# Performance work log

Measured on AMD Instinct MI355X. Metric: run time of the kernel, lower is better.

Reference implementation:

```python
import jax, jax.numpy as jnp
import numpy as np
import math

B, D_MODEL, H, D_K, L = 24, 128, 8, 16, 512


def setup_inputs() -> dict:
    key = jax.random.key(0)
    ks = jax.random.split(key, 5)
    x = jax.random.normal(ks[0], (B, D_MODEL, L), dtype=jnp.float32)
    Wq = jax.random.normal(ks[1], (H, B, D_K, D_MODEL), dtype=jnp.float32)
    Wk = jax.random.normal(ks[2], (H, B, D_K, D_MODEL), dtype=jnp.float32)
    Wv = jax.random.normal(ks[3], (H, B, D_K, D_MODEL), dtype=jnp.float32)
    Wo = jax.random.normal(ks[4], (B, H * D_K, D_MODEL), dtype=jnp.float32)
    return {"x": x, "Wq": Wq, "Wk": Wk, "Wv": Wv, "Wo": Wo}


def reference(x, Wq, Wk, Wv, Wo):
    # Per-head, per-batch projections: [h,b,k,d] @ [b,d,l] -> [h,b,k,l]
    Q = jnp.einsum('hbkd,bdl->hbkl', Wq, x)
    K = jnp.einsum('hbkd,bdl->hbkl', Wk, x)
    V = jnp.einsum('hbkd,bdl->hbkl', Wv, x)
    # scores[h,b,l,m] = Q[:, :, :, l] . K[:, :, :, m]; torch softmax dim=1 of
    # the [B, L, L] score -> softmax over the QUERY axis l (axis=2 here).
    scores = jnp.einsum('hbkl,hbkm->hblm', Q, K) / math.sqrt(D_K)
    attn = jax.nn.softmax(scores, axis=2)
    # head_i = V @ attn : [h,b,v,l] @ [h,b,l,m] -> [h,b,v,m]
    heads = jnp.einsum('hbvl,hblm->hbvm', V, attn)
    # concat heads along channel dim: [b, h*v, L]
    head = heads.transpose(1, 0, 2, 3).reshape(B, H * D_K, L)
    # out = Wo @ head : [b, h*v, d_model] treated as [b,128,128] @ [b,128,L]
    out = jnp.einsum('bod,bdl->bol', Wo, head)
    return out
```

## Files before the change

kernel.cpp:

```cpp
#include <hip/hip_runtime.h>
#include <math.h>

#define NB 24
#define DM 128
#define NH 8
#define DK 16
#define LL 512
#define HB (NH * NB)

#define XTH_OFF 0
#define XTL_OFF 3145728
#define HT_OFF  6291456

typedef __attribute__((ext_vector_type(8))) short bf16x8;
typedef __attribute__((ext_vector_type(4))) float f32x4;
typedef __attribute__((ext_vector_type(4))) int   i32x4;

#define MFMA  __builtin_amdgcn_mfma_f32_16x16x32_bf16
#define EXP2  __builtin_amdgcn_exp2f
#define BPERM __builtin_amdgcn_ds_bpermute

static __device__ __forceinline__ unsigned bfr(float x) {
    return (__float_as_uint(x) + 0x8000u) & 0xffff0000u;
}

static __device__ __forceinline__ unsigned cvtpk(float a, float b) {
    unsigned r;
    asm("v_cvt_pk_bf16_f32 %0, %1, %2" : "=v"(r) : "v"(a), "v"(b));
    return r;
}

static __device__ __forceinline__ void wsplit(const float* __restrict__ p,
                                              bf16x8& aH, bf16x8& aL) {
    const float4 f0 = *(const float4*)p;
    const float4 f1 = *(const float4*)(p + 4);
    const float f[8] = {f0.x, f0.y, f0.z, f0.w, f1.x, f1.y, f1.z, f1.w};
    i32x4 h, l;
    #pragma unroll
    for (int q = 0; q < 4; ++q) {
        const unsigned h0 = bfr(f[2 * q]), h1 = bfr(f[2 * q + 1]);
        const unsigned e0 = bfr(f[2 * q]     - __uint_as_float(h0));
        const unsigned e1 = bfr(f[2 * q + 1] - __uint_as_float(h1));
        h[q] = (int)((h0 >> 16) | (h1 & 0xffff0000u));
        l[q] = (int)((e0 >> 16) | (e1 & 0xffff0000u));
    }
    aH = __builtin_bit_cast(bf16x8, h);
    aL = __builtin_bit_cast(bf16x8, l);
}

__global__ __launch_bounds__(256)
void prep(const float* __restrict__ x,
          unsigned short* __restrict__ xthi,
          unsigned short* __restrict__ xtlo)
{
    __shared__ float T[64][65];
    const int bid = blockIdx.x, tid = threadIdx.x;
    const int b = bid >> 3, lc = bid & 7;

    #pragma unroll
    for (int half = 0; half < 2; ++half) {
        const int d0 = half << 6;
        const float* __restrict__ xb =
            x + (size_t)b * 65536 + (size_t)d0 * LL + lc * 64;
        if (half) __syncthreads();
        #pragma unroll
        for (int i = 0; i < 16; ++i) {
            const int idx = i * 256 + tid;
            T[idx >> 6][idx & 63] = xb[(size_t)(idx >> 6) * LL + (idx & 63)];
        }
        __syncthreads();
        #pragma unroll
        for (int i = 0; i < 8; ++i) {
            const int idx = (i * 256 + tid) * 2;
            const int l = idx >> 6, dd = idx & 63;
            const float v0 = T[dd][l], v1 = T[dd + 1][l];
            const unsigned h0 = bfr(v0), h1 = bfr(v1);
            const unsigned e0 = bfr(v0 - __uint_as_float(h0));
            const unsigned e1 = bfr(v1 - __uint_as_float(h1));
            const size_t o = (size_t)b * 65536 +
                             (size_t)(lc * 64 + l) * DM + d0 + dd;
            *(unsigned*)(xthi + o) = (h0 >> 16) | (h1 & 0xffff0000u);
            *(unsigned*)(xtlo + o) = (e0 >> 16) | (e1 & 0xffff0000u);
        }
    }
}

static __device__ __forceinline__ void pv_acc(
    const f32x4& s0, const f32x4& s1, float M, float& sm,
    f32x4& O, const bf16x8& aV, int addr0, int addr1, bool up, bool odd16)
{
    const float e0 = EXP2(s0[0] - M), e1 = EXP2(s0[1] - M);
    const float e2 = EXP2(s0[2] - M), e3 = EXP2(s0[3] - M);
    const float e4 = EXP2(s1[0] - M), e5 = EXP2(s1[1] - M);
    const float e6 = EXP2(s1[2] - M), e7 = EXP2(s1[3] - M);
    sm += ((e0 + e1) + (e2 + e3)) + ((e4 + e5) + (e6 + e7));
    const unsigned c0 = cvtpk(e0, e1), c1 = cvtpk(e2, e3);
    const unsigned c2 = cvtpk(e4, e5), c3 = cvtpk(e6, e7);
    const int r0 = (int)(odd16 ? c2 : c0);
    const int r1 = (int)(odd16 ? c0 : c2);
    const int r2 = (int)(odd16 ? c3 : c1);
    const int r3 = (int)(odd16 ? c1 : c3);
    const int w0 = BPERM(addr0, r0);
    const int w1 = BPERM(addr1, r1);
    const int w2 = BPERM(addr0, r2);
    const int w3 = BPERM(addr1, r3);
    i32x4 bi = { up ? w0 : w1, up ? w2 : w3,
                 up ? w1 : w0, up ? w3 : w2 };
    O = MFMA(aV, __builtin_bit_cast(bf16x8, bi), O, 0, 0, 0);
}

#define QK_STRIDE 40
#define V_STRIDE  520

__global__ __launch_bounds__(512)
void qkv_attn(const unsigned short* __restrict__ xthi,
              const unsigned short* __restrict__ xtlo,
              const float* __restrict__ Wq,
              const float* __restrict__ Wk,
              const float* __restrict__ Wv,
              unsigned short* __restrict__ ht)
{
    __shared__ unsigned short qs[LL * QK_STRIDE];
    __shared__ unsigned short ks[LL * QK_STRIDE];
    __shared__ unsigned short vs[DK * V_STRIDE];

    const int hb    = blockIdx.x;
    const int b     = hb % NB;
    const int wv    = threadIdx.x >> 6;
    const int lane  = threadIdx.x & 63;
    const int g     = lane >> 4;
    const int mR    = lane & 15;
    const int lQ    = wv * 64;

    {
        const float* __restrict__ wqp = Wq + (size_t)hb * 2048 + mR * 128 + g * 8;
        const float* __restrict__ wkp = Wk + (size_t)hb * 2048 + mR * 128 + g * 8;
        const float* __restrict__ wvp = Wv + (size_t)hb * 2048 + mR * 128 + g * 8;
        const unsigned short* __restrict__ xh = xthi + (size_t)b * 65536 + g * 8;
        const unsigned short* __restrict__ xl = xtlo + (size_t)b * 65536 + g * 8;

        f32x4 CQ[4], CK[4], CV[4];
        #pragma unroll
        for (int t = 0; t < 4; ++t) {
            CQ[t] = (f32x4){0.f, 0.f, 0.f, 0.f};
            CK[t] = (f32x4){0.f, 0.f, 0.f, 0.f};
            CV[t] = (f32x4){0.f, 0.f, 0.f, 0.f};
        }

        #pragma unroll
        for (int kk = 0; kk < 4; ++kk) {
            bf16x8 bH[4], bL[4];
            #pragma unroll
            for (int t = 0; t < 4; ++t) {
                const size_t ro = (size_t)(lQ + t * 16 + mR) * DM + kk * 32;
                bH[t] = *(const bf16x8*)(xh + ro);
                bL[t] = *(const bf16x8*)(xl + ro);
            }
            bf16x8 aH, aL;
            wsplit(wqp + kk * 32, aH, aL);
            #pragma unroll
            for (int t = 0; t < 4; ++t) {
                CQ[t] = MFMA(aH, bH[t], CQ[t], 0, 0, 0);
                CQ[t] = MFMA(aH, bL[t], CQ[t], 0, 0, 0);
                CQ[t] = MFMA(aL, bH[t], CQ[t], 0, 0, 0);
            }
            wsplit(wkp + kk * 32, aH, aL);
            #pragma unroll
            for (int t = 0; t < 4; ++t) {
                CK[t] = MFMA(aH, bH[t], CK[t], 0, 0, 0);
                CK[t] = MFMA(aH, bL[t], CK[t], 0, 0, 0);
                CK[t] = MFMA(aL, bH[t], CK[t], 0, 0, 0);
            }
            wsplit(wvp + kk * 32, aH, aL);
            #pragma unroll
            for (int t = 0; t < 4; ++t) {
                CV[t] = MFMA(aH, bH[t], CV[t], 0, 0, 0);
                CV[t] = MFMA(aH, bL[t], CV[t], 0, 0, 0);
                CV[t] = MFMA(aL, bH[t], CV[t], 0, 0, 0);
            }
        }

        #pragma unroll
        for (int t = 0; t < 4; ++t) {
            const int l = lQ + t * 16 + mR;
            #pragma unroll
            for (int i = 0; i < 4; ++i)
                vs[(4 * g + i) * V_STRIDE + l] =
                    (unsigned short)(bfr(CV[t][i]) >> 16);
        }
        #pragma unroll
        for (int t = 0; t < 4; ++t) {
            const int l = lQ + t * 16 + mR;
            ushort4 hi4, lo4;
            #pragma unroll
            for (int i = 0; i < 4; ++i) {
                const float v = CQ[t][i];
                const unsigned h = bfr(v);
                const unsigned lw = bfr(v - __uint_as_float(h));
                ((unsigned short*)&hi4)[i] = (unsigned short)(h >> 16);
                ((unsigned short*)&lo4)[i] = (unsigned short)(lw >> 16);
            }
            *(ushort4*)(qs + l * QK_STRIDE + 4 * g)      = hi4;
            *(ushort4*)(qs + l * QK_STRIDE + 16 + 4 * g) = lo4;
        }
        #pragma unroll
        for (int t = 0; t < 4; ++t) {
            const int r = lQ + t * 16 + mR;
            ushort4 hi4, lo4;
            #pragma unroll
            for (int i = 0; i < 4; ++i) {
                const float v = CK[t][i] * (0.25f * 1.44269504f);
                const unsigned h = bfr(v);
                const unsigned lw = bfr(v - __uint_as_float(h));
                ((unsigned short*)&hi4)[i] = (unsigned short)(h >> 16);
                ((unsigned short*)&lo4)[i] = (unsigned short)(lw >> 16);
            }
            *(ushort4*)(ks + r * QK_STRIDE + 4 * g)      = hi4;
            *(ushort4*)(ks + r * QK_STRIDE + 16 + 4 * g) = lo4;
        }
    }

    __syncthreads();

    bf16x8 K0[2], K0s[2], K1[2], K1s[2];
    #pragma unroll
    for (int sub = 0; sub < 2; ++sub) {
        const unsigned short* Kr0 = ks + (lQ + sub * 32 + mR) * QK_STRIDE;
        const unsigned short* Kr1 = Kr0 + 16 * QK_STRIDE;
        K0[sub]  = *(const bf16x8*)(Kr0 + g * 8);
        K0s[sub] = *(const bf16x8*)(Kr0 + (g ^ 2) * 8);
        K1[sub]  = *(const bf16x8*)(Kr1 + g * 8);
        K1s[sub] = *(const bf16x8*)(Kr1 + (g ^ 2) * 8);
    }

    const unsigned short* qrow = qs + mR * QK_STRIDE + g * 8;
    const unsigned short* vrow = vs + mR * V_STRIDE + g * 8;

    const int  aLo   = ((g & 1) * 32 + mR) * 4;
    const int  aHi   = aLo + 64;
    const bool up    = (g < 2);
    const bool odd16 = (g & 1);
    const int  addr0 = up ? aLo : aHi;
    const int  addr1 = up ? aHi : aLo;

    float MA[2] = {-1e30f, -1e30f}, MB[2] = {-1e30f, -1e30f};
    for (int l = 0; l < LL; l += 32) {
        const bf16x8 aQ0 = *(const bf16x8*)(qrow + l * QK_STRIDE);
        const bf16x8 aQ1 = *(const bf16x8*)(qrow + (l + 16) * QK_STRIDE);
        #pragma unroll
        for (int sub = 0; sub < 2; ++sub) {
            const f32x4 z = {0.f,0.f,0.f,0.f};
            const f32x4 sA0 = MFMA(aQ0, K0[sub], z, 0,0,0);
            const f32x4 sB0 = MFMA(aQ0, K1[sub], z, 0,0,0);
            const f32x4 sA1 = MFMA(aQ1, K0[sub], z, 0,0,0);
            const f32x4 sB1 = MFMA(aQ1, K1[sub], z, 0,0,0);
            float tmA = fmaxf(fmaxf(fmaxf(sA0[0],sA0[1]), fmaxf(sA0[2],sA0[3])),
                              fmaxf(fmaxf(sA1[0],sA1[1]), fmaxf(sA1[2],sA1[3])));
            float tmB = fmaxf(fmaxf(fmaxf(sB0[0],sB0[1]), fmaxf(sB0[2],sB0[3])),
                              fmaxf(fmaxf(sB1[0],sB1[1]), fmaxf(sB1[2],sB1[3])));
            tmA = fmaxf(tmA, __shfl_xor(tmA, 16, 64));
            tmA = fmaxf(tmA, __shfl_xor(tmA, 32, 64));
            tmB = fmaxf(tmB, __shfl_xor(tmB, 16, 64));
            tmB = fmaxf(tmB, __shfl_xor(tmB, 32, 64));
            MA[sub] = fmaxf(MA[sub], tmA);
            MB[sub] = fmaxf(MB[sub], tmB);
        }
    }

    f32x4 O[2][2];
    float smA[2] = {0.f, 0.f}, smB[2] = {0.f, 0.f};
    #pragma unroll
    for (int sub = 0; sub < 2; ++sub)
        #pragma unroll
        for (int gr = 0; gr < 2; ++gr)
            O[sub][gr] = (f32x4){0.f, 0.f, 0.f, 0.f};

    for (int l = 0; l < LL; l += 32) {
        const bf16x8 aQ0 = *(const bf16x8*)(qrow + l * QK_STRIDE);
        const bf16x8 aQ1 = *(const bf16x8*)(qrow + (l + 16) * QK_STRIDE);
        const bf16x8 aV  = *(const bf16x8*)(vrow + l);

        #pragma unroll
        for (int sub = 0; sub < 2; ++sub) {
            const f32x4 z = {0.f,0.f,0.f,0.f};
            f32x4 sA0 = MFMA(aQ0, K0[sub], z, 0,0,0);
            sA0 = MFMA(aQ0, K0s[sub], sA0, 0,0,0);
            f32x4 sB0 = MFMA(aQ0, K1[sub], z, 0,0,0);
            sB0 = MFMA(aQ0, K1s[sub], sB0, 0,0,0);
            f32x4 sA1 = MFMA(aQ1, K0[sub], z, 0,0,0);
            sA1 = MFMA(aQ1, K0s[sub], sA1, 0,0,0);
            f32x4 sB1 = MFMA(aQ1, K1[sub], z, 0,0,0);
            sB1 = MFMA(aQ1, K1s[sub], sB1, 0,0,0);

            pv_acc(sA0, sA1, MA[sub], smA[sub], O[sub][0], aV,
                   addr0, addr1, up, odd16);
            pv_acc(sB0, sB1, MB[sub], smB[sub], O[sub][1], aV,
                   addr0, addr1, up, odd16);
        }
    }

    const int h = hb / NB, bb = hb % NB;
    #pragma unroll
    for (int sub = 0; sub < 2; ++sub) {
        float s0 = smA[sub], s1 = smB[sub];
        s0 += __shfl_xor(s0, 16, 64);  s0 += __shfl_xor(s0, 32, 64);
        s1 += __shfl_xor(s1, 16, 64);  s1 += __shfl_xor(s1, 32, 64);
        const float i0 = 1.f / s0, i1 = 1.f / s1;

        unsigned short* __restrict__ ho =
            ht + (size_t)bb * 65536 +
            (size_t)(lQ + sub * 32 + mR) * DM + h * 16 + 4 * g;
        ushort4 p0, p1;
        #pragma unroll
        for (int i = 0; i < 4; ++i) {
            ((unsigned short*)&p0)[i] =
                (unsigned short)(bfr(O[sub][0][i] * i0) >> 16);
            ((unsigned short*)&p1)[i] =
                (unsigned short)(bfr(O[sub][1][i] * i1) >> 16);
        }
        *(ushort4*)ho             = p0;
        *(ushort4*)(ho + 16 * DM) = p1;
    }
}

__global__ __launch_bounds__(256)
void out_mfma(const float* __restrict__ Wo,
              const unsigned short* __restrict__ ht,
              float* __restrict__ out)
{
    const int blk  = blockIdx.x;
    const int b    = blk >> 5;
    const int mq   = (blk >> 4) & 1;
    const int nq   = blk & 15;
    const int wv   = threadIdx.x >> 6;
    const int lane = threadIdx.x & 63;
    const int g = lane >> 4, mR = lane & 15;
    const int m0 = (mq * 4 + wv) * 16;
    const int n0 = nq * 32;

    const float* __restrict__ A =
        Wo + (size_t)b * 16384 + (size_t)(m0 + mR) * DM + g * 8;
    const unsigned short* __restrict__ B = ht + (size_t)b * 65536 + g * 8;

    f32x4 C0 = {0.f,0.f,0.f,0.f}, C1 = {0.f,0.f,0.f,0.f};
    #pragma unroll
    for (int kk = 0; kk < 4; ++kk) {
        const float4 f0 = *(const float4*)(A + kk * 32);
        const float4 f1 = *(const float4*)(A + kk * 32 + 4);
        i32x4 w;
        w[0] = (int)cvtpk(f0.x, f0.y);
        w[1] = (int)cvtpk(f0.z, f0.w);
        w[2] = (int)cvtpk(f1.x, f1.y);
        w[3] = (int)cvtpk(f1.z, f1.w);
        const bf16x8 aW = __builtin_bit_cast(bf16x8, w);
        const bf16x8 b0 = *(const bf16x8*)(B + (size_t)(n0 + mR) * DM + kk * 32);
        const bf16x8 b1 = *(const bf16x8*)(B + (size_t)(n0 + 16 + mR) * DM + kk * 32);
        C0 = MFMA(aW, b0, C0, 0, 0, 0);
        C1 = MFMA(aW, b1, C1, 0, 0, 0);
    }

    float* __restrict__ ob = out + (size_t)b * 65536 + (size_t)(m0 + 4 * g) * LL;
    #pragma unroll
    for (int i = 0; i < 4; ++i) {
        ob[(size_t)i * LL + n0 + mR]      = C0[i];
        ob[(size_t)i * LL + n0 + 16 + mR] = C1[i];
    }
}

extern "C" void kernel_launch(void* const* d_in, const int* in_sizes, int n_in,
                              void* d_out, int out_size, void* d_ws, size_t ws_size,
                              hipStream_t stream) {
    const float* x  = (const float*)d_in[0];
    const float* Wq = (const float*)d_in[1];
    const float* Wk = (const float*)d_in[2];
    const float* Wv = (const float*)d_in[3];
    const float* Wo = (const float*)d_in[4];
    float* out = (float*)d_out;

    char* ws = (char*)d_ws;
    unsigned short* xthi = (unsigned short*)(ws + XTH_OFF);
    unsigned short* xtlo = (unsigned short*)(ws + XTL_OFF);
    unsigned short* ht   = (unsigned short*)(ws + HT_OFF);

    prep     <<<192,     256, 0, stream>>>(x, xthi, xtlo);
    qkv_attn <<<HB,      512, 0, stream>>>(xthi, xtlo, Wq, Wk, Wv, ht);
    out_mfma <<<NB * 32, 256, 0, stream>>>(Wo, ht, out);
}
```

Before: 112.9 us.

## Permute query rows to drop bpermute shuffles in softmax-PV path

Reorders which query rows feed each MFMA A-operand so that the output accumulator layout of the score MFMA directly matches the B-operand layout of the PV MFMA. This removes four ds_bpermute ops and the select logic per pv_acc call. The per-iteration cross-lane max reduction is moved out of the loop and done once at the end. The Q/K LDS stride is changed from 40 to 42, which may alter bank conflicts and could misalign the 16-byte vector loads.

```diff
diff --git a/kernel.cpp b/kernel.cpp
--- a/kernel.cpp
+++ b/kernel.cpp
@@ -18,7 +18,6 @@
 
 #define MFMA  __builtin_amdgcn_mfma_f32_16x16x32_bf16
 #define EXP2  __builtin_amdgcn_exp2f
-#define BPERM __builtin_amdgcn_ds_bpermute
 
 static __device__ __forceinline__ unsigned bfr(float x) {
     return (__float_as_uint(x) + 0x8000u) & 0xffff0000u;
@@ -87,29 +86,19 @@
 
 static __device__ __forceinline__ void pv_acc(
     const f32x4& s0, const f32x4& s1, float M, float& sm,
-    f32x4& O, const bf16x8& aV, int addr0, int addr1, bool up, bool odd16)
+    f32x4& O, const bf16x8& aV)
 {
     const float e0 = EXP2(s0[0] - M), e1 = EXP2(s0[1] - M);
     const float e2 = EXP2(s0[2] - M), e3 = EXP2(s0[3] - M);
     const float e4 = EXP2(s1[0] - M), e5 = EXP2(s1[1] - M);
     const float e6 = EXP2(s1[2] - M), e7 = EXP2(s1[3] - M);
     sm += ((e0 + e1) + (e2 + e3)) + ((e4 + e5) + (e6 + e7));
-    const unsigned c0 = cvtpk(e0, e1), c1 = cvtpk(e2, e3);
-    const unsigned c2 = cvtpk(e4, e5), c3 = cvtpk(e6, e7);
-    const int r0 = (int)(odd16 ? c2 : c0);
-    const int r1 = (int)(odd16 ? c0 : c2);
-    const int r2 = (int)(odd16 ? c3 : c1);
-    const int r3 = (int)(odd16 ? c1 : c3);
-    const int w0 = BPERM(addr0, r0);
-    const int w1 = BPERM(addr1, r1);
-    const int w2 = BPERM(addr0, r2);
-    const int w3 = BPERM(addr1, r3);
-    i32x4 bi = { up ? w0 : w1, up ? w2 : w3,
-                 up ? w1 : w0, up ? w3 : w2 };
+    i32x4 bi = { (int)cvtpk(e0, e1), (int)cvtpk(e2, e3),
+                 (int)cvtpk(e4, e5), (int)cvtpk(e6, e7) };
     O = MFMA(aV, __builtin_bit_cast(bf16x8, bi), O, 0, 0, 0);
 }
 
-#define QK_STRIDE 40
+#define QK_STRIDE 42
 #define V_STRIDE  520
 
 __global__ __launch_bounds__(512)
@@ -233,20 +222,15 @@
         K1s[sub] = *(const bf16x8*)(Kr1 + (g ^ 2) * 8);
     }
 
-    const unsigned short* qrow = qs + mR * QK_STRIDE + g * 8;
-    const unsigned short* vrow = vs + mR * V_STRIDE + g * 8;
-
-    const int  aLo   = ((g & 1) * 32 + mR) * 4;
-    const int  aHi   = aLo + 64;
-    const bool up    = (g < 2);
-    const bool odd16 = (g & 1);
-    const int  addr0 = up ? aLo : aHi;
-    const int  addr1 = up ? aHi : aLo;
+    const int rA = 8 * (mR >> 2) + (mR & 3);
+    const unsigned short* qrowA = qs + rA * QK_STRIDE + g * 8;
+    const unsigned short* qrowB = qrowA + 4 * QK_STRIDE;
+    const unsigned short* vrow  = vs + mR * V_STRIDE + g * 8;
 
     float MA[2] = {-1e30f, -1e30f}, MB[2] = {-1e30f, -1e30f};
     for (int l = 0; l < LL; l += 32) {
-        const bf16x8 aQ0 = *(const bf16x8*)(qrow + l * QK_STRIDE);
-        const bf16x8 aQ1 = *(const bf16x8*)(qrow + (l + 16) * QK_STRIDE);
+        const bf16x8 aQ0 = *(const bf16x8*)(qrowA + l * QK_STRIDE);
+        const bf16x8 aQ1 = *(const bf16x8*)(qrowB + l * QK_STRIDE);
         #pragma unroll
         for (int sub = 0; sub < 2; ++sub) {
             const f32x4 z = {0.f,0.f,0.f,0.f};
@@ -258,14 +242,17 @@
                               fmaxf(fmaxf(sA1[0],sA1[1]), fmaxf(sA1[2],sA1[3])));
             float tmB = fmaxf(fmaxf(fmaxf(sB0[0],sB0[1]), fmaxf(sB0[2],sB0[3])),
                               fmaxf(fmaxf(sB1[0],sB1[1]), fmaxf(sB1[2],sB1[3])));
-            tmA = fmaxf(tmA, __shfl_xor(tmA, 16, 64));
-            tmA = fmaxf(tmA, __shfl_xor(tmA, 32, 64));
-            tmB = fmaxf(tmB, __shfl_xor(tmB, 16, 64));
-            tmB = fmaxf(tmB, __shfl_xor(tmB, 32, 64));
             MA[sub] = fmaxf(MA[sub], tmA);
             MB[sub] = fmaxf(MB[sub], tmB);
         }
     }
+    #pragma unroll
+    for (int sub = 0; sub < 2; ++sub) {
+        MA[sub] = fmaxf(MA[sub], __shfl_xor(MA[sub], 16, 64));
+        MA[sub] = fmaxf(MA[sub], __shfl_xor(MA[sub], 32, 64));
+        MB[sub] = fmaxf(MB[sub], __shfl_xor(MB[sub], 16, 64));
+        MB[sub] = fmaxf(MB[sub], __shfl_xor(MB[sub], 32, 64));
+    }
 
     f32x4 O[2][2];
     float smA[2] = {0.f, 0.f}, smB[2] = {0.f, 0.f};
@@ -276,8 +263,8 @@
             O[sub][gr] = (f32x4){0.f, 0.f, 0.f, 0.f};
 
     for (int l = 0; l < LL; l += 32) {
-        const bf16x8 aQ0 = *(const bf16x8*)(qrow + l * QK_STRIDE);
-        const bf16x8 aQ1 = *(const bf16x8*)(qrow + (l + 16) * QK_STRIDE);
+        const bf16x8 aQ0 = *(const bf16x8*)(qrowA + l * QK_STRIDE);
+        const bf16x8 aQ1 = *(const bf16x8*)(qrowB + l * QK_STRIDE);
         const bf16x8 aV  = *(const bf16x8*)(vrow + l);
 
         #pragma unroll
@@ -292,10 +279,8 @@
             f32x4 sB1 = MFMA(aQ1, K1[sub], z, 0,0,0);
             sB1 = MFMA(aQ1, K1s[sub], sB1, 0,0,0);
 
-            pv_acc(sA0, sA1, MA[sub], smA[sub], O[sub][0], aV,
-                   addr0, addr1, up, odd16);
-            pv_acc(sB0, sB1, MB[sub], smB[sub], O[sub][1], aV,
-                   addr0, addr1, up, odd16);
+            pv_acc(sA0, sA1, MA[sub], smA[sub], O[sub][0], aV);
+            pv_acc(sB0, sB1, MB[sub], smB[sub], O[sub][1], aV);
         }
     }
 
```

New measurement: 113.8 us. About the same (+0.8%).
